# Performance work log

Measured on AMD Instinct MI355X. Metric: run time of the kernel, lower is better.

The kernel has to match this reference:

```python
import jax, jax.numpy as jnp
import numpy as np

S, B, D, H = 256, 32, 512, 512

def setup_inputs() -> dict:
    key = jax.random.key(0)
    ks = jax.random.split(key, 14)
    return {
        "x": jax.random.normal(ks[0], (S, B, D), jnp.float32),
        "hidden_prev": jax.random.normal(ks[1], (1, B, H), jnp.float32) * 0.1,
        "Z_state": jax.random.normal(ks[2], (1, B, H, D), jnp.float32) * 0.01,
        "F_state": jax.random.normal(ks[3], (1, B, H, D), jnp.float32) * 0.01,
        "wz_state": jax.random.normal(ks[4], (1, B, H), jnp.float32) * 0.01,
        "wf_state": jax.random.normal(ks[5], (1, B, H), jnp.float32) * 0.01,
        "bz_state": jax.random.normal(ks[6], (1, B, H), jnp.float32) * 0.01,
        "bf_state": jax.random.normal(ks[7], (1, B, H), jnp.float32) * 0.01,
        "wm_z": jax.random.normal(ks[8], (H, D), jnp.float32) * 0.1,
        "wm_f": jax.random.normal(ks[9], (H, D), jnp.float32) * 0.1,
        "wv_z": jax.random.normal(ks[10], (1, H), jnp.float32) * 0.1,
        "wv_f": jax.random.normal(ks[11], (1, H), jnp.float32) * 0.1,
        "bias_z": jax.random.normal(ks[12], (1, H), jnp.float32) * 0.1,
        "bias_f": jax.random.normal(ks[13], (1, H), jnp.float32) * 0.1,
    }

def reference(x, hidden_prev, Z_state, F_state, wz_state, wf_state, bz_state, bf_state,
              wm_z, wm_f, wv_z, wv_f, bias_z, bias_f):
    # Input projections for both gates, done once: [S,B,H]
    pre_z = jnp.einsum('sbd,hd->sbh', x, wm_z)
    pre_f = jnp.einsum('sbd,hd->sbh', x, wm_f)

    def step(carry, inp):
        cell, Z, Fm, wz, wf, bz, bf = carry
        x_t, pz, pf = inp  # [B,D], [B,H], [B,H]
        z = jnp.tanh(pz + wv_z * cell + bias_z)          # [B,H]
        f = jax.nn.sigmoid(pf + wv_f * cell + bias_f)    # [B,H]
        zf = (1.0 - f) * (1.0 - z * z)
        fz = (cell - z) * (1.0 - f) * f
        common = f + zf * wv_z + fz * wv_f
        # RTRL sensitivity updates (outer products over [B,H,D])
        Zn = common[..., None] * Z + zf[..., None] * x_t[:, None, :]
        Fn = common[..., None] * Fm + fz[..., None] * x_t[:, None, :]
        wzn = cell * zf + common * wz
        wfn = cell * fz + common * wf
        bzn = zf + common * bz
        bfn = fz + common * bf
        new_cell = cell * f + (1.0 - f) * z
        return (new_cell, Zn, Fn, wzn, wfn, bzn, bfn), new_cell

    carry0 = (hidden_prev[0], Z_state[0], F_state[0],
              wz_state[0], wf_state[0], bz_state[0], bf_state[0])
    carry, cells = jax.lax.scan(step, carry0, (x, pre_z, pre_f))
    new_cell, Zn, Fn, wzn, wfn, bzn, bfn = carry
    return (cells, new_cell[None], Zn[None], Fn[None],
            wzn[None], wfn[None], bzn[None], bfn[None])
```

## Files before the change

kernel.cpp:

```cpp
#include <hip/hip_runtime.h>
#include <math.h>

namespace {

typedef short short8 __attribute__((ext_vector_type(8)));
typedef float floatx4 __attribute__((ext_vector_type(4)));
typedef unsigned int uint32;
typedef unsigned short u16;
typedef unsigned long long u64;

constexpr int S = 256, B = 32, D = 512, H = 512;
constexpr int BH = B * H;
constexpr int M1 = S * B;
constexpr int WN = H * D;
constexpr int SBH = S * BH;

__device__ __forceinline__ int swz(int row, int col8) {
  return row * 64 + (col8 ^ ((row & 7) << 3));
}

__device__ __forceinline__ uint32 f2bf(float f) {
  uint32 x = __float_as_uint(f);
  return (x + 0x7fffu + ((x >> 16) & 1u)) >> 16;
}

__device__ __forceinline__ float fast_sigmoid(float x) {
  float e = __expf(-x);
  return __builtin_amdgcn_rcpf(1.0f + e);
}
__device__ __forceinline__ float fast_tanh(float x) {
  float e = __expf(-2.0f * x);
  return fmaf(2.0f, __builtin_amdgcn_rcpf(1.0f + e), -1.0f);
}

__global__ __launch_bounds__(256) void convert_w(
    const float* __restrict__ wmz, const float* __restrict__ wmf,
    u16* __restrict__ wmzb, u16* __restrict__ wmfb) {
  int i = (blockIdx.x * 256 + threadIdx.x) * 8;
  const float* src;
  u16* dst;
  int off;
  if (i < WN) {
    src = wmz; dst = wmzb; off = i;
  } else {
    src = wmf; dst = wmfb; off = i - WN;
  }
  float4 a = *(const float4*)&src[off];
  float4 b = *(const float4*)&src[off + 4];
  uint4 o;
  o.x = f2bf(a.x) | (f2bf(a.y) << 16);
  o.y = f2bf(a.z) | (f2bf(a.w) << 16);
  o.z = f2bf(b.x) | (f2bf(b.y) << 16);
  o.w = f2bf(b.z) | (f2bf(b.w) << 16);
  *(uint4*)&dst[off] = o;
}

__global__ __launch_bounds__(256) void xpose_kernel(
    const float* __restrict__ x, u16* __restrict__ XT) {
  __shared__ float lds[64][65];
  const int s0 = blockIdx.x * 64;
  const int d0 = blockIdx.y * 64;
  const int b = blockIdx.z;
  const int r = threadIdx.x >> 4;
  const int c4 = (threadIdx.x & 15) * 4;
#pragma unroll
  for (int p = 0; p < 4; ++p) {
    const int rr = r + p * 16;
    float4 v = *(const float4*)&x[(size_t)(s0 + rr) * (B * D) +
                                  (size_t)b * D + d0 + c4];
    lds[c4 + 0][rr] = v.x;
    lds[c4 + 1][rr] = v.y;
    lds[c4 + 2][rr] = v.z;
    lds[c4 + 3][rr] = v.w;
  }
  __syncthreads();
#pragma unroll
  for (int p = 0; p < 4; ++p) {
    const int dr = r + p * 16;
    const float v0 = lds[dr][c4 + 0];
    const float v1 = lds[dr][c4 + 1];
    const float v2 = lds[dr][c4 + 2];
    const float v3 = lds[dr][c4 + 3];
    u64 o = (u64)f2bf(v0) | ((u64)f2bf(v1) << 16) | ((u64)f2bf(v2) << 32) |
            ((u64)f2bf(v3) << 48);
    *(u64*)&XT[((size_t)b * D + d0 + dr) * S + s0 + c4] = o;
  }
}

__global__ __launch_bounds__(256) void proj_gemm(
    const float* __restrict__ x, const u16* __restrict__ wmzb,
    const u16* __restrict__ wmfb, float2* __restrict__ pzf) {
  __shared__ u16 As[128 * 64];
  __shared__ u16 Bzs[64 * 64];
  __shared__ u16 Bfs[64 * 64];
  const int tid = threadIdx.x;
  const int m0 = blockIdx.x * 128;
  const int n0 = blockIdx.y * 64;
  const int w = tid >> 6, l = tid & 63;
  const int lr = l & 15, lg = l >> 4;
  floatx4 accz[2][4], accf[2][4];
#pragma unroll
  for (int m = 0; m < 2; ++m)
#pragma unroll
    for (int n = 0; n < 4; ++n) {
      accz[m][n] = 0;
      accf[m][n] = 0;
    }
  const int sr = tid >> 3;
  const int sc = (tid & 7) * 8;
  for (int k0 = 0; k0 < D; k0 += 64) {
    __syncthreads();
#pragma unroll
    for (int p = 0; p < 4; ++p) {
      const int r = sr + 32 * p;
      const float* xp = &x[(size_t)(m0 + r) * D + k0 + sc];
      float4 a = *(const float4*)xp;
      float4 b = *(const float4*)(xp + 4);
      uint4 o;
      o.x = f2bf(a.x) | (f2bf(a.y) << 16);
      o.y = f2bf(a.z) | (f2bf(a.w) << 16);
      o.z = f2bf(b.x) | (f2bf(b.y) << 16);
      o.w = f2bf(b.z) | (f2bf(b.w) << 16);
      *(uint4*)&As[swz(r, sc)] = o;
    }
#pragma unroll
    for (int p = 0; p < 2; ++p) {
      const int r = sr + 32 * p;
      *(short8*)&Bzs[swz(r, sc)] =
          *(const short8*)&wmzb[(size_t)(n0 + r) * D + k0 + sc];
      *(short8*)&Bfs[swz(r, sc)] =
          *(const short8*)&wmfb[(size_t)(n0 + r) * D + k0 + sc];
    }
    __syncthreads();
#pragma unroll
    for (int kk = 0; kk < 2; ++kk) {
      const int kb = kk * 32 + lg * 8;
      short8 a0 = *(const short8*)&As[swz(32 * w + lr, kb)];
      short8 a1 = *(const short8*)&As[swz(32 * w + 16 + lr, kb)];
#pragma unroll
      for (int n = 0; n < 4; ++n) {
        short8 bz = *(const short8*)&Bzs[swz(16 * n + lr, kb)];
        short8 bf = *(const short8*)&Bfs[swz(16 * n + lr, kb)];
        accz[0][n] = __builtin_amdgcn_mfma_f32_16x16x32_bf16(a0, bz, accz[0][n], 0, 0, 0);
        accz[1][n] = __builtin_amdgcn_mfma_f32_16x16x32_bf16(a1, bz, accz[1][n], 0, 0, 0);
        accf[0][n] = __builtin_amdgcn_mfma_f32_16x16x32_bf16(a0, bf, accf[0][n], 0, 0, 0);
        accf[1][n] = __builtin_amdgcn_mfma_f32_16x16x32_bf16(a1, bf, accf[1][n], 0, 0, 0);
      }
    }
  }
#pragma unroll
  for (int m = 0; m < 2; ++m)
#pragma unroll
    for (int n = 0; n < 4; ++n)
#pragma unroll
      for (int j = 0; j < 4; ++j) {
        int row = m0 + 32 * w + 16 * m + lg * 4 + j;
        int col = n0 + 16 * n + lr;
        pzf[(size_t)row * H + col] = make_float2(accz[m][n][j], accf[m][n][j]);
      }
}

#define STEP_BODY(J)                                                       \
    const float z = fast_tanh(fmaf(wvz, cell, pzv));                       \
    const float f = fast_sigmoid(fmaf(wvf, cell, pfv));                    \
    const float zf = (1.0f - f) * (1.0f - z * z);                          \
    const float fz = (cell - z) * (1.0f - f) * f;                          \
    const float common = f + zf * wvz + fz * wvf;                          \
    wz = fmaf(common, wz, cell * zf);                                      \
    wf = fmaf(common, wf, cell * fz);                                      \
    bz = fmaf(common, bz, zf);                                             \
    bf = fmaf(common, bf, fz);                                             \
    cell = fmaf(f, cell - z, z);                                           \
    const size_t ti = (size_t)(t0 + (J)) * BH;                             \
    cp[ti] = cell;                                                         \
    pz[ti] = make_float2(                                                  \
        __uint_as_float(f2bf(zf) | (f2bf(fz) << 16)), common);

#define STEP_L(J, Q)                                                       \
  {                                                                        \
    const float pzv = Q.x + bsz, pfv = Q.y + bsf;                          \
    Q = pz[(size_t)(t0 + 16 + (J)) * BH];                                  \
    STEP_BODY(J)                                                           \
  }

#define STEP_N(J, Q)                                                       \
  {                                                                        \
    const float pzv = Q.x + bsz, pfv = Q.y + bsf;                          \
    STEP_BODY(J)                                                           \
  }

__global__ __launch_bounds__(64, 1) void scan_fwd(
    const float* __restrict__ hidden_prev, const float* __restrict__ wz0,
    const float* __restrict__ wf0, const float* __restrict__ bz0,
    const float* __restrict__ bf0, const float* __restrict__ wvz_,
    const float* __restrict__ wvf_, const float* __restrict__ bsz_,
    const float* __restrict__ bsf_, float2* pzf_,
    float* __restrict__ out_cells, float* __restrict__ out_newcell,
    float* __restrict__ out_wzn, float* __restrict__ out_wfn,
    float* __restrict__ out_bzn, float* __restrict__ out_bfn) {
  const int bh = blockIdx.x * 64 + threadIdx.x;
  const int h = bh & (H - 1);
  float cell = hidden_prev[bh];
  float wz = wz0[bh], wf = wf0[bh], bz = bz0[bh], bf = bf0[bh];
  const float wvz = wvz_[h], wvf = wvf_[h], bsz = bsz_[h], bsf = bsf_[h];
  float2* pz = pzf_ + bh;
  float* cp = out_cells + bh;

  float2 q0 = pz[(size_t)0 * BH], q1 = pz[(size_t)1 * BH];
  float2 q2 = pz[(size_t)2 * BH], q3 = pz[(size_t)3 * BH];
  float2 q4 = pz[(size_t)4 * BH], q5 = pz[(size_t)5 * BH];
  float2 q6 = pz[(size_t)6 * BH], q7 = pz[(size_t)7 * BH];
  float2 q8 = pz[(size_t)8 * BH], q9 = pz[(size_t)9 * BH];
  float2 q10 = pz[(size_t)10 * BH], q11 = pz[(size_t)11 * BH];
  float2 q12 = pz[(size_t)12 * BH], q13 = pz[(size_t)13 * BH];
  float2 q14 = pz[(size_t)14 * BH], q15 = pz[(size_t)15 * BH];

  for (int t0 = 0; t0 < S - 16; t0 += 16) {
    STEP_L(0, q0)  STEP_L(1, q1)  STEP_L(2, q2)  STEP_L(3, q3)
    STEP_L(4, q4)  STEP_L(5, q5)  STEP_L(6, q6)  STEP_L(7, q7)
    STEP_L(8, q8)  STEP_L(9, q9)  STEP_L(10, q10) STEP_L(11, q11)
    STEP_L(12, q12) STEP_L(13, q13) STEP_L(14, q14) STEP_L(15, q15)
  }
  {
    const int t0 = S - 16;
    STEP_N(0, q0)  STEP_N(1, q1)  STEP_N(2, q2)  STEP_N(3, q3)
    STEP_N(4, q4)  STEP_N(5, q5)  STEP_N(6, q6)  STEP_N(7, q7)
    STEP_N(8, q8)  STEP_N(9, q9)  STEP_N(10, q10) STEP_N(11, q11)
    STEP_N(12, q12) STEP_N(13, q13) STEP_N(14, q14) STEP_N(15, q15)
  }
  out_newcell[bh] = cell;
  out_wzn[bh] = wz;
  out_wfn[bh] = wf;
  out_bzn[bh] = bz;
  out_bfn[bh] = bf;
}

__global__ __launch_bounds__(1024) void suffix_kernel(
    const float2* __restrict__ pzfc, u16* __restrict__ AzT,
    u16* __restrict__ AfT, float* __restrict__ P0_out) {
  __shared__ float prods[16][65];
  __shared__ uint32 tl[S * 65];
  const int bh_l = threadIdx.x & 63;
  const int c = threadIdx.x >> 6;
  const int bh = blockIdx.x * 64 + bh_l;
  const float2* p = pzfc + bh;
  float2 v[16];
#pragma unroll
  for (int i = 0; i < 16; ++i) v[i] = p[(size_t)(c * 16 + i) * BH];
  float L = 1.0f;
#pragma unroll
  for (int i = 0; i < 16; ++i) L *= v[i].y;
  prods[c][bh_l] = L;
  __syncthreads();
  float run = 1.0f;
#pragma unroll
  for (int cc = 1; cc < 16; ++cc)
    if (cc > c) run *= prods[cc][bh_l];
#pragma unroll
  for (int i = 15; i >= 0; --i) {
    const int t = c * 16 + i;
    const uint32 w32 = __float_as_uint(v[i].x);
    const float zf = __uint_as_float((w32 & 0xffffu) << 16);
    const float fz = __uint_as_float(w32 & 0xffff0000u);
    tl[t * 65 + bh_l] = f2bf(zf * run) | (f2bf(fz * run) << 16);
    run *= v[i].y;
  }
  if (c == 0) P0_out[bh] = run;
  __syncthreads();
  const size_t base = (size_t)blockIdx.x * 64 * S;
#pragma unroll
  for (int it = 0; it < 4; ++it) {
    const int qi = it * 1024 + threadIdx.x;
    const int r = qi >> 6;
    const int qt = (qi & 63) * 4;
    const uint32 a0 = tl[(qt + 0) * 65 + r];
    const uint32 a1 = tl[(qt + 1) * 65 + r];
    const uint32 a2 = tl[(qt + 2) * 65 + r];
    const uint32 a3 = tl[(qt + 3) * 65 + r];
    u64 lo = (u64)(a0 & 0xffffu) | ((u64)(a1 & 0xffffu) << 16) |
             ((u64)(a2 & 0xffffu) << 32) | ((u64)(a3 & 0xffffu) << 48);
    u64 hi = (u64)(a0 >> 16) | ((u64)(a1 >> 16) << 16) |
             ((u64)(a2 >> 16) << 32) | ((u64)(a3 >> 16) << 48);
    *(u64*)&AzT[base + (size_t)r * S + qt] = lo;
    *(u64*)&AfT[base + (size_t)r * S + qt] = hi;
  }
}

__global__ __launch_bounds__(256, 2) void out_gemm(
    const u16* __restrict__ AzT, const u16* __restrict__ AfT,
    const u16* __restrict__ XT, const float* __restrict__ P0,
    const float* __restrict__ Z0, const float* __restrict__ F0,
    float* __restrict__ Zn, float* __restrict__ Fn) {
  __shared__ u16 Azs[2][128 * 64];
  __shared__ u16 Afs[2][128 * 64];
  __shared__ u16 Xs[2][64 * 64];
  const int tid = threadIdx.x;
  const int h0 = blockIdx.x * 128;
  const int d0 = blockIdx.y * 64;
  const int b = blockIdx.z;
  const u16* Az = AzT + (size_t)b * H * S;
  const u16* Af = AfT + (size_t)b * H * S;
  const u16* Xb = XT + (size_t)b * D * S;
  const int w = tid >> 6, l = tid & 63;
  const int lr = l & 15, lg = l >> 4;
  floatx4 accz[2][4], accf[2][4];
#pragma unroll
  for (int m = 0; m < 2; ++m)
#pragma unroll
    for (int n = 0; n < 4; ++n) {
      accz[m][n] = 0;
      accf[m][n] = 0;
    }
  const int sr = tid >> 3;
  const int sc = (tid & 7) * 8;

  short8 rA[4], rF[4], rX[2];

#define OG_LOAD(T0)                                                        \
  {                                                                        \
    _Pragma("unroll") for (int p = 0; p < 4; ++p) {                        \
      const int r = sr + 32 * p;                                           \
      rA[p] = *(const short8*)&Az[(size_t)(h0 + r) * S + (T0) + sc];       \
      rF[p] = *(const short8*)&Af[(size_t)(h0 + r) * S + (T0) + sc];       \
    }                                                                      \
    _Pragma("unroll") for (int p = 0; p < 2; ++p) {                        \
      const int r = sr + 32 * p;                                           \
      rX[p] = *(const short8*)&Xb[(size_t)(d0 + r) * S + (T0) + sc];       \
    }                                                                      \
  }

#define OG_WRITE(BUF)                                                      \
  {                                                                        \
    _Pragma("unroll") for (int p = 0; p < 4; ++p) {                        \
      const int r = sr + 32 * p;                                           \
      *(short8*)&Azs[BUF][swz(r, sc)] = rA[p];                             \
      *(short8*)&Afs[BUF][swz(r, sc)] = rF[p];                             \
    }                                                                      \
    _Pragma("unroll") for (int p = 0; p < 2; ++p) {                        \
      const int r = sr + 32 * p;                                           \
      *(short8*)&Xs[BUF][swz(r, sc)] = rX[p];                              \
    }                                                                      \
  }

#define OG_COMPUTE(BUF)                                                    \
  _Pragma("unroll") for (int kk = 0; kk < 2; ++kk) {                       \
    const int kb = kk * 32 + lg * 8;                                       \
    short8 az0 = *(const short8*)&Azs[BUF][swz(32 * w + lr, kb)];          \
    short8 az1 = *(const short8*)&Azs[BUF][swz(32 * w + 16 + lr, kb)];     \
    short8 af0 = *(const short8*)&Afs[BUF][swz(32 * w + lr, kb)];          \
    short8 af1 = *(const short8*)&Afs[BUF][swz(32 * w + 16 + lr, kb)];     \
    _Pragma("unroll") for (int n = 0; n < 4; ++n) {                        \
      short8 xf = *(const short8*)&Xs[BUF][swz(16 * n + lr, kb)];          \
      accz[0][n] = __builtin_amdgcn_mfma_f32_16x16x32_bf16(az0, xf, accz[0][n], 0, 0, 0); \
      accz[1][n] = __builtin_amdgcn_mfma_f32_16x16x32_bf16(az1, xf, accz[1][n], 0, 0, 0); \
      accf[0][n] = __builtin_amdgcn_mfma_f32_16x16x32_bf16(af0, xf, accf[0][n], 0, 0, 0); \
      accf[1][n] = __builtin_amdgcn_mfma_f32_16x16x32_bf16(af1, xf, accf[1][n], 0, 0, 0); \
    }                                                                      \
  }

  OG_LOAD(0)
  OG_WRITE(0)
  __syncthreads();
  OG_LOAD(64)
  OG_COMPUTE(0)
  OG_WRITE(1)
  __syncthreads();
  OG_LOAD(128)
  OG_COMPUTE(1)
  OG_WRITE(0)
  __syncthreads();
  OG_LOAD(192)
  OG_COMPUTE(0)
  OG_WRITE(1)
  __syncthreads();
  OG_COMPUTE(1)

#pragma unroll
  for (int m = 0; m < 2; ++m)
#pragma unroll
    for (int j = 0; j < 4; ++j) {
      const int row = h0 + 32 * w + 16 * m + lg * 4 + j;
      const float p0 = P0[b * H + row];
#pragma unroll
      for (int n = 0; n < 4; ++n) {
        const int col = d0 + 16 * n + lr;
        const size_t idx = ((size_t)b * H + row) * D + col;
        Zn[idx] = fmaf(p0, Z0[idx], accz[m][n][j]);
        Fn[idx] = fmaf(p0, F0[idx], accf[m][n][j]);
      }
    }
#undef OG_LOAD
#undef OG_WRITE
#undef OG_COMPUTE
}

}

extern "C" void kernel_launch(void* const* d_in, const int* in_sizes, int n_in,
                              void* d_out, int out_size, void* d_ws,
                              size_t ws_size, hipStream_t stream) {
  const float* x = (const float*)d_in[0];
  const float* hidden_prev = (const float*)d_in[1];
  const float* Z_state = (const float*)d_in[2];
  const float* F_state = (const float*)d_in[3];
  const float* wz_state = (const float*)d_in[4];
  const float* wf_state = (const float*)d_in[5];
  const float* bz_state = (const float*)d_in[6];
  const float* bf_state = (const float*)d_in[7];
  const float* wm_z = (const float*)d_in[8];
  const float* wm_f = (const float*)d_in[9];
  const float* wv_z = (const float*)d_in[10];
  const float* wv_f = (const float*)d_in[11];
  const float* bias_z = (const float*)d_in[12];
  const float* bias_f = (const float*)d_in[13];

  float2* pzf = (float2*)d_ws;
  u16* AzT = (u16*)(pzf + SBH);
  u16* AfT = AzT + SBH;
  u16* XT = AfT + SBH;
  u16* wmzb = XT + SBH;
  u16* wmfb = wmzb + WN;
  float* P0 = (float*)(wmfb + WN);

  float* out = (float*)d_out;
  float* out_cells = out;
  float* out_newcell = out + SBH;
  float* out_Zn = out_newcell + BH;
  float* out_Fn = out_Zn + (size_t)BH * D;
  float* out_wzn = out_Fn + (size_t)BH * D;
  float* out_wfn = out_wzn + BH;
  float* out_bzn = out_wfn + BH;
  float* out_bfn = out_bzn + BH;

  convert_w<<<2 * WN / 8 / 256, 256, 0, stream>>>(wm_z, wm_f, wmzb, wmfb);
  xpose_kernel<<<dim3(S / 64, D / 64, B), 256, 0, stream>>>(x, XT);
  proj_gemm<<<dim3(M1 / 128, H / 64), 256, 0, stream>>>(x, wmzb, wmfb, pzf);
  scan_fwd<<<BH / 64, 64, 0, stream>>>(
      hidden_prev, wz_state, wf_state, bz_state, bf_state, wv_z, wv_f, bias_z,
      bias_f, pzf, out_cells, out_newcell, out_wzn, out_wfn, out_bzn,
      out_bfn);
  suffix_kernel<<<BH / 64, 1024, 0, stream>>>(pzf, AzT, AfT, P0);
  out_gemm<<<dim3(H / 128, D / 64, B), 256, 0, stream>>>(
      AzT, AfT, XT, P0, Z_state, F_state, out_Zn, out_Fn);
}
```

Measured before the change: 105.4 us.

## Single-buffer out_gemm LDS tiles to raise occupancy to four blocks per CU

Replaces the double-buffered LDS tiles in out_gemm with single buffers, halving shared memory per block from 80KB to 40KB. The launch bound is raised to 4 blocks per CU. Extra barriers are added between compute and the next LDS write so the single buffer is not overwritten while still being read. The aim is to hide global load latency through more resident blocks instead of intra-block double buffering, at the cost of more synchronisation and a tighter register budget.

```diff
diff --git a/kernel.cpp b/kernel.cpp
--- a/kernel.cpp
+++ b/kernel.cpp
@@ -286,14 +286,14 @@
   }
 }
 
-__global__ __launch_bounds__(256, 2) void out_gemm(
+__global__ __launch_bounds__(256, 4) void out_gemm(
     const u16* __restrict__ AzT, const u16* __restrict__ AfT,
     const u16* __restrict__ XT, const float* __restrict__ P0,
     const float* __restrict__ Z0, const float* __restrict__ F0,
     float* __restrict__ Zn, float* __restrict__ Fn) {
-  __shared__ u16 Azs[2][128 * 64];
-  __shared__ u16 Afs[2][128 * 64];
-  __shared__ u16 Xs[2][64 * 64];
+  __shared__ u16 Azs[128 * 64];
+  __shared__ u16 Afs[128 * 64];
+  __shared__ u16 Xs[64 * 64];
   const int tid = threadIdx.x;
   const int h0 = blockIdx.x * 128;
   const int d0 = blockIdx.y * 64;
@@ -329,28 +329,28 @@
     }                                                                      \
   }
 
-#define OG_WRITE(BUF)                                                      \
+#define OG_WRITE()                                                         \
   {                                                                        \
     _Pragma("unroll") for (int p = 0; p < 4; ++p) {                        \
       const int r = sr + 32 * p;                                           \
-      *(short8*)&Azs[BUF][swz(r, sc)] = rA[p];                             \
-      *(short8*)&Afs[BUF][swz(r, sc)] = rF[p];                             \
+      *(short8*)&Azs[swz(r, sc)] = rA[p];                                  \
+      *(short8*)&Afs[swz(r, sc)] = rF[p];                                  \
     }                                                                      \
     _Pragma("unroll") for (int p = 0; p < 2; ++p) {                        \
       const int r = sr + 32 * p;                                           \
-      *(short8*)&Xs[BUF][swz(r, sc)] = rX[p];                              \
+      *(short8*)&Xs[swz(r, sc)] = rX[p];                                   \
     }                                                                      \
   }
 
-#define OG_COMPUTE(BUF)                                                    \
+#define OG_COMPUTE()                                                       \
   _Pragma("unroll") for (int kk = 0; kk < 2; ++kk) {                       \
     const int kb = kk * 32 + lg * 8;                                       \
-    short8 az0 = *(const short8*)&Azs[BUF][swz(32 * w + lr, kb)];          \
-    short8 az1 = *(const short8*)&Azs[BUF][swz(32 * w + 16 + lr, kb)];     \
-    short8 af0 = *(const short8*)&Afs[BUF][swz(32 * w + lr, kb)];          \
-    short8 af1 = *(const short8*)&Afs[BUF][swz(32 * w + 16 + lr, kb)];     \
+    short8 az0 = *(const short8*)&Azs[swz(32 * w + lr, kb)];               \
+    short8 az1 = *(const short8*)&Azs[swz(32 * w + 16 + lr, kb)];          \
+    short8 af0 = *(const short8*)&Afs[swz(32 * w + lr, kb)];               \
+    short8 af1 = *(const short8*)&Afs[swz(32 * w + 16 + lr, kb)];          \
     _Pragma("unroll") for (int n = 0; n < 4; ++n) {                        \
-      short8 xf = *(const short8*)&Xs[BUF][swz(16 * n + lr, kb)];          \
+      short8 xf = *(const short8*)&Xs[swz(16 * n + lr, kb)];               \
       accz[0][n] = __builtin_amdgcn_mfma_f32_16x16x32_bf16(az0, xf, accz[0][n], 0, 0, 0); \
       accz[1][n] = __builtin_amdgcn_mfma_f32_16x16x32_bf16(az1, xf, accz[1][n], 0, 0, 0); \
       accf[0][n] = __builtin_amdgcn_mfma_f32_16x16x32_bf16(af0, xf, accf[0][n], 0, 0, 0); \
@@ -359,21 +359,24 @@
   }
 
   OG_LOAD(0)
-  OG_WRITE(0)
+  OG_WRITE()
   __syncthreads();
   OG_LOAD(64)
-  OG_COMPUTE(0)
-  OG_WRITE(1)
+  OG_COMPUTE()
+  __syncthreads();
+  OG_WRITE()
   __syncthreads();
   OG_LOAD(128)
-  OG_COMPUTE(1)
-  OG_WRITE(0)
+  OG_COMPUTE()
+  __syncthreads();
+  OG_WRITE()
   __syncthreads();
   OG_LOAD(192)
-  OG_COMPUTE(0)
-  OG_WRITE(1)
-  __syncthreads();
-  OG_COMPUTE(1)
+  OG_COMPUTE()
+  __syncthreads();
+  OG_WRITE()
+  __syncthreads();
+  OG_COMPUTE()
 
 #pragma unroll
   for (int m = 0; m < 2; ++m)
```

Result: slower. 132.6 us (+25.8%).

## Split out_gemm into separate Z/F blocks and stage epilogue through LDS for vector stores

Applied to the files above, without the earlier changes.

The output GEMM now assigns the Z and F sensitivity outputs to separate blocks, doubling the grid along z. This halves accumulators and shared memory per block and raises launch bounds to 3 blocks per CU. The epilogue first writes accumulators to LDS, then each thread does coalesced float4 reads of the old state and float4 writes of the result, replacing scattered scalar accesses. In exchange the X tile is loaded twice, once by each of the two blocks, and the kernel gains an extra LDS round trip and two extra barriers.

```diff
diff --git a/kernel.cpp b/kernel.cpp
--- a/kernel.cpp
+++ b/kernel.cpp
@@ -286,42 +286,38 @@
   }
 }
 
-__global__ __launch_bounds__(256, 2) void out_gemm(
+__global__ __launch_bounds__(256, 3) void out_gemm(
     const u16* __restrict__ AzT, const u16* __restrict__ AfT,
     const u16* __restrict__ XT, const float* __restrict__ P0,
     const float* __restrict__ Z0, const float* __restrict__ F0,
     float* __restrict__ Zn, float* __restrict__ Fn) {
-  __shared__ u16 Azs[2][128 * 64];
-  __shared__ u16 Afs[2][128 * 64];
-  __shared__ u16 Xs[2][64 * 64];
+  __shared__ u16 smem[2][(128 + 64) * 64];
   const int tid = threadIdx.x;
   const int h0 = blockIdx.x * 128;
   const int d0 = blockIdx.y * 64;
-  const int b = blockIdx.z;
-  const u16* Az = AzT + (size_t)b * H * S;
-  const u16* Af = AfT + (size_t)b * H * S;
+  const int bz = blockIdx.z;
+  const int b = bz >> 1;
+  const u16* A = ((bz & 1) ? AfT : AzT) + (size_t)b * H * S;
+  const float* C0 = (bz & 1) ? F0 : Z0;
+  float* Cn = (bz & 1) ? Fn : Zn;
   const u16* Xb = XT + (size_t)b * D * S;
   const int w = tid >> 6, l = tid & 63;
   const int lr = l & 15, lg = l >> 4;
-  floatx4 accz[2][4], accf[2][4];
+  floatx4 acc[2][4];
 #pragma unroll
   for (int m = 0; m < 2; ++m)
 #pragma unroll
-    for (int n = 0; n < 4; ++n) {
-      accz[m][n] = 0;
-      accf[m][n] = 0;
-    }
+    for (int n = 0; n < 4; ++n) acc[m][n] = 0;
   const int sr = tid >> 3;
   const int sc = (tid & 7) * 8;
 
-  short8 rA[4], rF[4], rX[2];
+  short8 rA[4], rX[2];
 
 #define OG_LOAD(T0)                                                        \
   {                                                                        \
     _Pragma("unroll") for (int p = 0; p < 4; ++p) {                        \
       const int r = sr + 32 * p;                                           \
-      rA[p] = *(const short8*)&Az[(size_t)(h0 + r) * S + (T0) + sc];       \
-      rF[p] = *(const short8*)&Af[(size_t)(h0 + r) * S + (T0) + sc];       \
+      rA[p] = *(const short8*)&A[(size_t)(h0 + r) * S + (T0) + sc];        \
     }                                                                      \
     _Pragma("unroll") for (int p = 0; p < 2; ++p) {                        \
       const int r = sr + 32 * p;                                           \
@@ -331,30 +327,31 @@
 
 #define OG_WRITE(BUF)                                                      \
   {                                                                        \
+    u16* As_ = smem[BUF];                                                  \
+    u16* Xs_ = smem[BUF] + 128 * 64;                                       \
     _Pragma("unroll") for (int p = 0; p < 4; ++p) {                        \
       const int r = sr + 32 * p;                                           \
-      *(short8*)&Azs[BUF][swz(r, sc)] = rA[p];                             \
-      *(short8*)&Afs[BUF][swz(r, sc)] = rF[p];                             \
+      *(short8*)&As_[swz(r, sc)] = rA[p];                                  \
     }                                                                      \
     _Pragma("unroll") for (int p = 0; p < 2; ++p) {                        \
       const int r = sr + 32 * p;                                           \
-      *(short8*)&Xs[BUF][swz(r, sc)] = rX[p];                              \
+      *(short8*)&Xs_[swz(r, sc)] = rX[p];                                  \
     }                                                                      \
   }
 
 #define OG_COMPUTE(BUF)                                                    \
-  _Pragma("unroll") for (int kk = 0; kk < 2; ++kk) {                       \
-    const int kb = kk * 32 + lg * 8;                                       \
-    short8 az0 = *(const short8*)&Azs[BUF][swz(32 * w + lr, kb)];          \
-    short8 az1 = *(const short8*)&Azs[BUF][swz(32 * w + 16 + lr, kb)];     \
-    short8 af0 = *(const short8*)&Afs[BUF][swz(32 * w + lr, kb)];          \
-    short8 af1 = *(const short8*)&Afs[BUF][swz(32 * w + 16 + lr, kb)];     \
-    _Pragma("unroll") for (int n = 0; n < 4; ++n) {                        \
-      short8 xf = *(const short8*)&Xs[BUF][swz(16 * n + lr, kb)];          \
-      accz[0][n] = __builtin_amdgcn_mfma_f32_16x16x32_bf16(az0, xf, accz[0][n], 0, 0, 0); \
-      accz[1][n] = __builtin_amdgcn_mfma_f32_16x16x32_bf16(az1, xf, accz[1][n], 0, 0, 0); \
-      accf[0][n] = __builtin_amdgcn_mfma_f32_16x16x32_bf16(af0, xf, accf[0][n], 0, 0, 0); \
-      accf[1][n] = __builtin_amdgcn_mfma_f32_16x16x32_bf16(af1, xf, accf[1][n], 0, 0, 0); \
+  {                                                                        \
+    const u16* As_ = smem[BUF];                                            \
+    const u16* Xs_ = smem[BUF] + 128 * 64;                                 \
+    _Pragma("unroll") for (int kk = 0; kk < 2; ++kk) {                     \
+      const int kb = kk * 32 + lg * 8;                                     \
+      short8 a0 = *(const short8*)&As_[swz(32 * w + lr, kb)];              \
+      short8 a1 = *(const short8*)&As_[swz(32 * w + 16 + lr, kb)];         \
+      _Pragma("unroll") for (int n = 0; n < 4; ++n) {                      \
+        short8 xf = *(const short8*)&Xs_[swz(16 * n + lr, kb)];            \
+        acc[0][n] = __builtin_amdgcn_mfma_f32_16x16x32_bf16(a0, xf, acc[0][n], 0, 0, 0); \
+        acc[1][n] = __builtin_amdgcn_mfma_f32_16x16x32_bf16(a1, xf, acc[1][n], 0, 0, 0); \
+      }                                                                    \
     }                                                                      \
   }
 
@@ -375,20 +372,35 @@
   __syncthreads();
   OG_COMPUTE(1)
 
+  __syncthreads();
+  float* eps = (float*)&smem[0][0];
 #pragma unroll
   for (int m = 0; m < 2; ++m)
 #pragma unroll
-    for (int j = 0; j < 4; ++j) {
-      const int row = h0 + 32 * w + 16 * m + lg * 4 + j;
-      const float p0 = P0[b * H + row];
-#pragma unroll
-      for (int n = 0; n < 4; ++n) {
-        const int col = d0 + 16 * n + lr;
-        const size_t idx = ((size_t)b * H + row) * D + col;
-        Zn[idx] = fmaf(p0, Z0[idx], accz[m][n][j]);
-        Fn[idx] = fmaf(p0, F0[idx], accf[m][n][j]);
+    for (int n = 0; n < 4; ++n)
+#pragma unroll
+      for (int j = 0; j < 4; ++j) {
+        const int row = 32 * w + 16 * m + lg * 4 + j;
+        eps[row * 68 + 16 * n + lr] = acc[m][n][j];
       }
-    }
+  __syncthreads();
+#pragma unroll
+  for (int i = 0; i < 8; ++i) {
+    const int id = i * 256 + tid;
+    const int row = id >> 4;
+    const int c4 = (id & 15) * 4;
+    const int h = h0 + row;
+    const float p0 = P0[b * H + h];
+    const size_t gi = ((size_t)b * H + h) * D + d0 + c4;
+    const float4 a = *(const float4*)&eps[row * 68 + c4];
+    const float4 c0 = *(const float4*)&C0[gi];
+    float4 o;
+    o.x = fmaf(p0, c0.x, a.x);
+    o.y = fmaf(p0, c0.y, a.y);
+    o.z = fmaf(p0, c0.z, a.z);
+    o.w = fmaf(p0, c0.w, a.w);
+    *(float4*)&Cn[gi] = o;
+  }
 #undef OG_LOAD
 #undef OG_WRITE
 #undef OG_COMPUTE
@@ -440,6 +452,6 @@
       bias_f, pzf, out_cells, out_newcell, out_wzn, out_wfn, out_bzn,
       out_bfn);
   suffix_kernel<<<BH / 64, 1024, 0, stream>>>(pzf, AzT, AfT, P0);
-  out_gemm<<<dim3(H / 128, D / 64, B), 256, 0, stream>>>(
+  out_gemm<<<dim3(H / 128, D / 64, B * 2), 256, 0, stream>>>(
       AzT, AfT, XT, P0, Z_state, F_state, out_Zn, out_Fn);
 }
```

Result: no change. 105.5 us (+0.1%).
